# Kernel tuning notes

Measured on AMD Instinct MI355X. Metric: run time of the kernel, lower is better.

Reference implementation:

```python
import jax, jax.numpy as jnp
import numpy as np

K = 16  # number of neighbors (init kwarg k)


def setup_inputs() -> dict:
    key = jax.random.key(0)
    k1, k2 = jax.random.split(key)
    B, N, D, F = 2, 2048, 16, 64
    points = jax.random.normal(k1, (B, N, D), dtype=jnp.float32)
    features = jax.random.normal(k2, (B, N, F), dtype=jnp.float32)
    return {"features": features, "points": points}


def reference(features, points):
    # points: [B, N, D]
    B, N, _ = points.shape
    # Pairwise Euclidean distances via broadcasted subtraction, matching
    # tf.norm(points[:, :, None] - points[:, None, :], axis=-1): [B, N, N]
    diff = points[:, :, None, :] - points[:, None, :, :]
    distance = jnp.sqrt(jnp.sum(diff * diff, axis=-1))
    # top (k+1) smallest distances == top_k of negated distance; drop self (col 0)
    _, topk_indices = jax.lax.top_k(-distance, K + 1)  # [B, N, K+1] int32
    topk_indices = topk_indices[:, :, 1:]               # [B, N, K]
    batch_indices = jnp.broadcast_to(
        jnp.arange(B, dtype=jnp.int32)[:, None, None, None], (B, N, K, 1)
    )
    # [B, N, K, 2] -> (batch_idx, neighbor_idx) pairs for gather_nd-style use
    return jnp.concatenate([batch_indices, topk_indices[..., None]], axis=3)
```

## Files before the change

### kernel.cpp

```cpp
#include <hip/hip_runtime.h>
#include <stdint.h>


#define NPTS 2048
#define DIMS 16
#define KK 16
#define THREADS 256
#define NQ 4
#define CPT (NPTS / THREADS)
#define PER_LANE (NPTS / 64)
#define RUNS 4
#define RLEN 8

__device__ __forceinline__ void ce(uint64_t& a, uint64_t& b) {
    uint64_t lo = (a < b) ? a : b;
    uint64_t hi = (a < b) ? b : a;
    a = lo; b = hi;
}

__global__ __launch_bounds__(THREADS, 4) void knn_kernel(
    const float* __restrict__ points, int* __restrict__ out)
{
    const int qbase = blockIdx.x * NQ;
    const int b = qbase >> 11;
    const float* bp = points + (size_t)b * NPTS * DIMS;

    __shared__ float dist[NQ][NPTS];

    const int tid = threadIdx.x;

    float qp[NQ][DIMS];
#pragma unroll
    for (int w = 0; w < NQ; ++w) {
        const int n = (qbase + w) & (NPTS - 1);
        const float4* qp4 = (const float4*)(bp + (size_t)n * DIMS);
#pragma unroll
        for (int v = 0; v < 4; ++v) {
            float4 t = qp4[v];
            qp[w][4 * v + 0] = t.x; qp[w][4 * v + 1] = t.y;
            qp[w][4 * v + 2] = t.z; qp[w][4 * v + 3] = t.w;
        }
    }

#pragma unroll 2
    for (int i = 0; i < CPT; ++i) {
        const int c = tid + i * THREADS;
        const float4* cp4 = (const float4*)(bp + (size_t)c * DIMS);
        float cv[DIMS];
#pragma unroll
        for (int v = 0; v < 4; ++v) {
            float4 t = cp4[v];
            cv[4 * v + 0] = t.x; cv[4 * v + 1] = t.y;
            cv[4 * v + 2] = t.z; cv[4 * v + 3] = t.w;
        }
#pragma unroll
        for (int w = 0; w < NQ; ++w) {
            float s[DIMS];
#pragma unroll
            for (int d = 0; d < DIMS; ++d) {
                float df = qp[w][d] - cv[d];
                s[d] = __fmul_rn(df, df);
            }
            float r0 = __fadd_rn(s[0], s[8]);
            float r1 = __fadd_rn(s[1], s[9]);
            float r2 = __fadd_rn(s[2], s[10]);
            float r3 = __fadd_rn(s[3], s[11]);
            float r4 = __fadd_rn(s[4], s[12]);
            float r5 = __fadd_rn(s[5], s[13]);
            float r6 = __fadd_rn(s[6], s[14]);
            float r7 = __fadd_rn(s[7], s[15]);
            float t0 = __fadd_rn(r0, r1);
            float t1 = __fadd_rn(r2, r3);
            float t2 = __fadd_rn(r4, r5);
            float t3 = __fadd_rn(r6, r7);
            float d2 = __fadd_rn(__fadd_rn(t0, t1), __fadd_rn(t2, t3));
            dist[w][c] = __fsqrt_rn(d2);
        }
    }
    __syncthreads();

    const int w = tid >> 6;
    const int lane = tid & 63;

    uint64_t k[PER_LANE];
#pragma unroll
    for (int j = 0; j < PER_LANE; ++j) {
        const int c = lane + 64 * j;
        k[j] = ((uint64_t)__float_as_uint(dist[w][c]) << 32) | (uint32_t)c;
    }

#pragma unroll
    for (int r = 0; r < RUNS; ++r) {
        uint64_t* p = k + r * RLEN;
        ce(p[0], p[1]); ce(p[2], p[3]); ce(p[4], p[5]); ce(p[6], p[7]);
        ce(p[0], p[2]); ce(p[1], p[3]); ce(p[4], p[6]); ce(p[5], p[7]);
        ce(p[1], p[2]); ce(p[5], p[6]);
        ce(p[0], p[4]); ce(p[1], p[5]); ce(p[2], p[6]); ce(p[3], p[7]);
        ce(p[1], p[4]); ce(p[3], p[6]);
        ce(p[2], p[4]); ce(p[3], p[5]);
        ce(p[3], p[4]);
    }

    for (int r = 0; r <= KK; ++r) {
        uint64_t m = k[0]; int hm = 0;
        if (k[8]  < m) { m = k[8];  hm = 1; }
        if (k[16] < m) { m = k[16]; hm = 2; }
        if (k[24] < m) { m = k[24]; hm = 3; }
        uint64_t g = m;
#pragma unroll
        for (int off = 1; off < 64; off <<= 1) {
            uint64_t o = (uint64_t)__shfl_xor((unsigned long long)g, off, 64);
            if (o < g) g = o;
        }
        if (m == g) {
            if (r > 0) {
                int2 val;
                val.x = b;
                val.y = (int)(uint32_t)(g & 0xffffffffu);
                *(int2*)(out + (((size_t)(qbase + w) * KK) + (size_t)(r - 1)) * 2) = val;
            }
#pragma unroll
            for (int h = 0; h < RUNS; ++h) {
                if (hm == h) {
#pragma unroll
                    for (int j = 0; j < RLEN - 1; ++j) k[h * RLEN + j] = k[h * RLEN + j + 1];
                    k[h * RLEN + RLEN - 1] = ~0ull;
                }
            }
        }
    }
}

extern "C" void kernel_launch(void* const* d_in, const int* in_sizes, int n_in,
                              void* d_out, int out_size, void* d_ws, size_t ws_size,
                              hipStream_t stream) {
    (void)d_ws; (void)ws_size; (void)out_size;
    const float* points;
    if (n_in >= 2 && in_sizes[1] == 2 * 2048 * 16) {
        points = (const float*)d_in[1];
    } else if (n_in >= 1 && in_sizes[0] == 2 * 2048 * 16) {
        points = (const float*)d_in[0];
    } else {
        points = (const float*)d_in[n_in - 1];
    }
    int* out = (int*)d_out;
    knn_kernel<<<(2 * 2048) / NQ, THREADS, 0, stream>>>(points, out);
}
```

Measured before the change: 86.99 us.

## Split each query across two waves with register top-k and merge-path combine

Each block now handles one query with two waves. Each wave computes distances for half the candidates directly into registers, so the shared distance array and the barrier between phases are gone. Each wave selects its own 17 smallest using a DPP-based wave min reduction in place of shfl_xor. The two sorted lists are then merged in shared memory by rank counting. This removes LDS traffic and shortens the per-wave selection, but every block now reloads all candidate points for a single query, losing the reuse across four queries per block.

```diff
diff --git a/kernel.cpp b/kernel.cpp
--- a/kernel.cpp
+++ b/kernel.cpp
@@ -5,12 +5,8 @@
 #define NPTS 2048
 #define DIMS 16
 #define KK 16
-#define THREADS 256
-#define NQ 4
-#define CPT (NPTS / THREADS)
-#define PER_LANE (NPTS / 64)
-#define RUNS 4
-#define RLEN 8
+#define THREADS 128
+#define CPL 16
 
 __device__ __forceinline__ void ce(uint64_t& a, uint64_t& b) {
     uint64_t lo = (a < b) ? a : b;
@@ -18,80 +14,94 @@
     a = lo; b = hi;
 }
 
+__device__ __forceinline__ uint64_t wave_min_u64(uint64_t v) {
+    uint32_t lo = (uint32_t)v;
+    uint32_t hi = (uint32_t)(v >> 32);
+#define DPP_STEP(CTRL, RMASK)                                                   \
+    {                                                                           \
+        uint32_t slo = (uint32_t)__builtin_amdgcn_update_dpp(                   \
+            -1, (int)lo, (CTRL), (RMASK), 0xF, false);                          \
+        uint32_t shi = (uint32_t)__builtin_amdgcn_update_dpp(                   \
+            -1, (int)hi, (CTRL), (RMASK), 0xF, false);                          \
+        bool lt = (shi < hi) || ((shi == hi) && (slo < lo));                    \
+        lo = lt ? slo : lo;                                                     \
+        hi = lt ? shi : hi;                                                     \
+    }
+    DPP_STEP(0x111, 0xF);
+    DPP_STEP(0x112, 0xF);
+    DPP_STEP(0x114, 0xF);
+    DPP_STEP(0x118, 0xF);
+    DPP_STEP(0x142, 0xA);
+    DPP_STEP(0x143, 0xC);
+#undef DPP_STEP
+    uint32_t glo = (uint32_t)__builtin_amdgcn_readlane((int)lo, 63);
+    uint32_t ghi = (uint32_t)__builtin_amdgcn_readlane((int)hi, 63);
+    return ((uint64_t)ghi << 32) | glo;
+}
+
 __global__ __launch_bounds__(THREADS, 4) void knn_kernel(
     const float* __restrict__ points, int* __restrict__ out)
 {
-    const int qbase = blockIdx.x * NQ;
-    const int b = qbase >> 11;
+    const int q = blockIdx.x;
+    const int b = q >> 11;
+    const int n = q & (NPTS - 1);
     const float* bp = points + (size_t)b * NPTS * DIMS;
 
-    __shared__ float dist[NQ][NPTS];
+    __shared__ uint64_t lists[2][KK + 1];
 
     const int tid = threadIdx.x;
+    const int wave = tid >> 6;
+    const int lane = tid & 63;
 
-    float qp[NQ][DIMS];
-#pragma unroll
-    for (int w = 0; w < NQ; ++w) {
-        const int n = (qbase + w) & (NPTS - 1);
+    float qp[DIMS];
+    {
         const float4* qp4 = (const float4*)(bp + (size_t)n * DIMS);
 #pragma unroll
         for (int v = 0; v < 4; ++v) {
             float4 t = qp4[v];
-            qp[w][4 * v + 0] = t.x; qp[w][4 * v + 1] = t.y;
-            qp[w][4 * v + 2] = t.z; qp[w][4 * v + 3] = t.w;
+            qp[4 * v + 0] = t.x; qp[4 * v + 1] = t.y;
+            qp[4 * v + 2] = t.z; qp[4 * v + 3] = t.w;
         }
     }
 
-#pragma unroll 2
-    for (int i = 0; i < CPT; ++i) {
-        const int c = tid + i * THREADS;
+    uint64_t k[CPL];
+#pragma unroll
+    for (int j = 0; j < CPL; ++j) {
+        const int c = (wave << 10) + lane + (j << 6);
         const float4* cp4 = (const float4*)(bp + (size_t)c * DIMS);
-        float cv[DIMS];
+        float s[DIMS];
 #pragma unroll
         for (int v = 0; v < 4; ++v) {
             float4 t = cp4[v];
-            cv[4 * v + 0] = t.x; cv[4 * v + 1] = t.y;
-            cv[4 * v + 2] = t.z; cv[4 * v + 3] = t.w;
+            float d0 = qp[4 * v + 0] - t.x;
+            float d1 = qp[4 * v + 1] - t.y;
+            float d2_ = qp[4 * v + 2] - t.z;
+            float d3 = qp[4 * v + 3] - t.w;
+            s[4 * v + 0] = __fmul_rn(d0, d0);
+            s[4 * v + 1] = __fmul_rn(d1, d1);
+            s[4 * v + 2] = __fmul_rn(d2_, d2_);
+            s[4 * v + 3] = __fmul_rn(d3, d3);
         }
-#pragma unroll
-        for (int w = 0; w < NQ; ++w) {
-            float s[DIMS];
-#pragma unroll
-            for (int d = 0; d < DIMS; ++d) {
-                float df = qp[w][d] - cv[d];
-                s[d] = __fmul_rn(df, df);
-            }
-            float r0 = __fadd_rn(s[0], s[8]);
-            float r1 = __fadd_rn(s[1], s[9]);
-            float r2 = __fadd_rn(s[2], s[10]);
-            float r3 = __fadd_rn(s[3], s[11]);
-            float r4 = __fadd_rn(s[4], s[12]);
-            float r5 = __fadd_rn(s[5], s[13]);
-            float r6 = __fadd_rn(s[6], s[14]);
-            float r7 = __fadd_rn(s[7], s[15]);
-            float t0 = __fadd_rn(r0, r1);
-            float t1 = __fadd_rn(r2, r3);
-            float t2 = __fadd_rn(r4, r5);
-            float t3 = __fadd_rn(r6, r7);
-            float d2 = __fadd_rn(__fadd_rn(t0, t1), __fadd_rn(t2, t3));
-            dist[w][c] = __fsqrt_rn(d2);
-        }
-    }
-    __syncthreads();
-
-    const int w = tid >> 6;
-    const int lane = tid & 63;
-
-    uint64_t k[PER_LANE];
-#pragma unroll
-    for (int j = 0; j < PER_LANE; ++j) {
-        const int c = lane + 64 * j;
-        k[j] = ((uint64_t)__float_as_uint(dist[w][c]) << 32) | (uint32_t)c;
+        float r0 = __fadd_rn(s[0], s[8]);
+        float r1 = __fadd_rn(s[1], s[9]);
+        float r2 = __fadd_rn(s[2], s[10]);
+        float r3 = __fadd_rn(s[3], s[11]);
+        float r4 = __fadd_rn(s[4], s[12]);
+        float r5 = __fadd_rn(s[5], s[13]);
+        float r6 = __fadd_rn(s[6], s[14]);
+        float r7 = __fadd_rn(s[7], s[15]);
+        float t0 = __fadd_rn(r0, r1);
+        float t1 = __fadd_rn(r2, r3);
+        float t2 = __fadd_rn(r4, r5);
+        float t3 = __fadd_rn(r6, r7);
+        float d2 = __fadd_rn(__fadd_rn(t0, t1), __fadd_rn(t2, t3));
+        float dist = __fsqrt_rn(d2);
+        k[j] = ((uint64_t)__float_as_uint(dist) << 32) | (uint32_t)c;
     }
 
 #pragma unroll
-    for (int r = 0; r < RUNS; ++r) {
-        uint64_t* p = k + r * RLEN;
+    for (int r = 0; r < 2; ++r) {
+        uint64_t* p = k + r * 8;
         ce(p[0], p[1]); ce(p[2], p[3]); ce(p[4], p[5]); ce(p[6], p[7]);
         ce(p[0], p[2]); ce(p[1], p[3]); ce(p[4], p[6]); ce(p[5], p[7]);
         ce(p[1], p[2]); ce(p[5], p[6]);
@@ -102,31 +112,36 @@
     }
 
     for (int r = 0; r <= KK; ++r) {
-        uint64_t m = k[0]; int hm = 0;
-        if (k[8]  < m) { m = k[8];  hm = 1; }
-        if (k[16] < m) { m = k[16]; hm = 2; }
-        if (k[24] < m) { m = k[24]; hm = 3; }
-        uint64_t g = m;
+        const bool a_min = k[0] < k[8];
+        const uint64_t m = a_min ? k[0] : k[8];
+        const uint64_t g = wave_min_u64(m);
+        if (m == g) {
+            lists[wave][r] = g;
+            if (a_min) {
 #pragma unroll
-        for (int off = 1; off < 64; off <<= 1) {
-            uint64_t o = (uint64_t)__shfl_xor((unsigned long long)g, off, 64);
-            if (o < g) g = o;
+                for (int j = 0; j < 7; ++j) k[j] = k[j + 1];
+                k[7] = ~0ull;
+            } else {
+#pragma unroll
+                for (int j = 8; j < 15; ++j) k[j] = k[j + 1];
+                k[15] = ~0ull;
+            }
         }
-        if (m == g) {
-            if (r > 0) {
-                int2 val;
-                val.x = b;
-                val.y = (int)(uint32_t)(g & 0xffffffffu);
-                *(int2*)(out + (((size_t)(qbase + w) * KK) + (size_t)(r - 1)) * 2) = val;
-            }
+    }
+    __syncthreads();
+
+    if (lane <= KK) {
+        const uint64_t mine = lists[wave][lane];
+        const uint64_t* other = lists[wave ^ 1];
+        int cnt = 0;
 #pragma unroll
-            for (int h = 0; h < RUNS; ++h) {
-                if (hm == h) {
-#pragma unroll
-                    for (int j = 0; j < RLEN - 1; ++j) k[h * RLEN + j] = k[h * RLEN + j + 1];
-                    k[h * RLEN + RLEN - 1] = ~0ull;
-                }
-            }
+        for (int t = 0; t <= KK; ++t) cnt += (other[t] < mine) ? 1 : 0;
+        const int rank = lane + cnt;
+        if (rank >= 1 && rank <= KK) {
+            int2 val;
+            val.x = b;
+            val.y = (int)(uint32_t)(mine & 0xffffffffu);
+            *(int2*)(out + (((size_t)q * KK) + (size_t)(rank - 1)) * 2) = val;
         }
     }
 }
@@ -144,5 +159,5 @@
         points = (const float*)d_in[n_in - 1];
     }
     int* out = (int*)d_out;
-    knn_kernel<<<(2 * 2048) / NQ, THREADS, 0, stream>>>(points, out);
+    knn_kernel<<<2 * 2048, THREADS, 0, stream>>>(points, out);
 }
```

Measured after the change: 94.28 us. 8.4% more time.
